# Kernel tuning notes

Hardware: AMD Instinct MI355X
Metric: run time of the kernel (lower is better)

## Reference

```python
import jax, jax.numpy as jnp
import numpy as np

IC = 256   # inter_channels
CIN = 512  # in_channels == out_channels
HOP = 3
EPS = 1e-5


def conv1x1(x, w, b):
    # x: [B,C,H,W], w: [O,C], b: [O]
    return jnp.einsum('bchw,oc->bohw', x, w) + b[None, :, None, None]


def bn_eval(x, g, beta, mean, var):
    inv = g / jnp.sqrt(var + EPS)
    return x * inv[None, :, None, None] + (beta - mean * inv)[None, :, None, None]


def setup_inputs() -> dict:
    key = jax.random.key(0)
    ks = jax.random.split(key, 12)
    s = lambda *sh: 0.02
    inp = {
        'x': jax.random.normal(ks[0], (4, CIN, 64, 64), dtype=jnp.float32),
        'delta': jnp.array([0.5], dtype=jnp.float32),
        'w1_w': jax.random.normal(ks[1], (IC, CIN), dtype=jnp.float32) * 0.02,
        'w1_b': jnp.zeros((IC,), jnp.float32),
        'bn1_g': jnp.ones((IC,), jnp.float32),
        'bn1_b': jnp.zeros((IC,), jnp.float32),
        'bn1_m': jnp.zeros((IC,), jnp.float32),
        'bn1_v': jnp.ones((IC,), jnp.float32),
        'node_w': jax.random.normal(ks[2], (IC, CIN), dtype=jnp.float32) * 0.02,
        'node_b': jnp.zeros((IC,), jnp.float32),
        'hop_w': jax.random.normal(ks[3], (HOP, IC, IC), dtype=jnp.float32) * 0.02,
        'hop_b': jnp.zeros((HOP, IC), jnp.float32),
        'fuse_w': jax.random.normal(ks[4], (IC, HOP * IC), dtype=jnp.float32) * 0.02,
        'fuse_b': jnp.zeros((IC,), jnp.float32),
        'bnf_g': jnp.ones((IC,), jnp.float32),
        'bnf_b': jnp.zeros((IC,), jnp.float32),
        'bnf_m': jnp.zeros((IC,), jnp.float32),
        'bnf_v': jnp.ones((IC,), jnp.float32),
        'res_w': jax.random.normal(ks[5], (CIN, 2 * IC), dtype=jnp.float32) * 0.02,
        'res_b': jnp.zeros((CIN,), jnp.float32),
        'bnr_g': jnp.ones((CIN,), jnp.float32),
        'bnr_b': jnp.zeros((CIN,), jnp.float32),
        'bnr_m': jnp.zeros((CIN,), jnp.float32),
        'bnr_v': jnp.ones((CIN,), jnp.float32),
    }
    return inp


def reference(x, delta, w1_w, w1_b, bn1_g, bn1_b, bn1_m, bn1_v,
              node_w, node_b, hop_w, hop_b, fuse_w, fuse_b,
              bnf_g, bnf_b, bnf_m, bnf_v, res_w, res_b,
              bnr_g, bnr_b, bnr_m, bnr_v):
    B, C, H, W = x.shape
    N = H * W
    # w1_conv == w2_conv (shared weights in the original module)
    wfeat = bn_eval(conv1x1(x, w1_w, w1_b), bn1_g, bn1_b, bn1_m, bn1_v)  # [B,IC,H,W]
    wflat = wfeat.reshape(B, IC, N)
    # initial_w = w1^T @ w2, scaled: [B,N,N]
    iw = jnp.einsum('bcn,bcm->bnm', wflat, wflat) * (IC ** -0.5)
    nodes = conv1x1(x, node_w, node_b).reshape(B, IC, N).transpose(0, 2, 1)  # [B,N,IC]
    # thresholded binary mask (non-differentiable, as in torch .ge)
    b0 = (jax.nn.sigmoid(iw) - delta[0] >= 0.0).astype(iw.dtype)
    bh = b0
    hops = []
    for i in range(HOP):
        s = jax.nn.softmax(bh * iw, axis=-1)          # [B,N,N]
        t = jnp.einsum('bnm,bmc->bnc', s, nodes)      # [B,N,IC]
        t = t.transpose(0, 2, 1).reshape(B, IC, H, W)
        t = conv1x1(t, hop_w[i], hop_b[i])
        hops.append(t)
        if i != HOP - 1:
            bh = jnp.matmul(bh, b0)                   # binary adjacency power
    x_p = jnp.concatenate(hops, axis=1)               # [B,HOP*IC,H,W]
    x_p = bn_eval(conv1x1(x_p, fuse_w, fuse_b), bnf_g, bnf_b, bnf_m, bnf_v)
    out = jnp.concatenate((wfeat * 0 + wfeat, x_p), axis=1) if False else jnp.concatenate((x_pad(x), x_p), axis=1)
    out = bn_eval(conv1x1(out, res_w, res_b), bnr_g, bnr_b, bnr_m, bnr_v)
    return out


def x_pad(x):
    # note: res_conv expects 2*IC input channels; original concatenates x (in_channels)
    # with x_p (inter_channels). With in_channels=512 and IC=256 the torch module as
    # written requires in_channels + IC == 2*IC only if in_channels == IC; the repo's
    # res_conv takes 2*inter_channels, so faithfully we feed x projected? No -- the
    # original concatenates raw x. To keep channel math consistent with the declared
    # Conv2d(2*IC, out), we slice x to IC channels (matches runnable configuration).
    return x[:, :IC]
```

## Files before the change

### kernel.cpp

```cpp
#include <hip/hip_runtime.h>

#define CINCH 512
#define ICH 256
#define NP 4096
#define BB 4
#define GSTRIDE ((size_t)NP*16)

typedef __attribute__((ext_vector_type(8))) short bf16x8;
typedef __attribute__((ext_vector_type(8))) unsigned short u16x8;
typedef __attribute__((ext_vector_type(4))) float f32x4;
typedef __attribute__((ext_vector_type(4))) int i32x4;
typedef unsigned short u16;
typedef unsigned char u8;
typedef unsigned long long u64;

__device__ __forceinline__ u16 f2bf(float f){
  unsigned u = __builtin_bit_cast(unsigned, f);
  u += 0x7FFFu + ((u>>16)&1u);
  return (u16)(u>>16);
}

__device__ __forceinline__ float b0_thr(float dv){
  if (dv <= 0.f) return -3.4e38f;
  if (dv >= 1.f) return  3.4e38f;
  return (float)log((double)dv/(1.0-(double)dv));
}

__device__ __forceinline__ size_t fragaddr(int row, int k){
  return (size_t)(row>>4)*GSTRIDE + (size_t)(k>>4)*256 + (size_t)((row&15)*16 + (k&15));
}
__device__ __forceinline__ size_t fragidx(int row, int col){
  return ((size_t)(row>>4)*(NP>>4) + (size_t)(col>>4))*256 + (size_t)((row&15)*16 + (col&15));
}
__device__ __forceinline__ size_t ndfrag(int ic, int n){
  return ((size_t)(ic>>4)*(NP>>5) + (size_t)(n>>5))*512
       + (size_t)((ic&15)*32 + ((n>>3)&3)*8 + (n&7));
}

__global__ __launch_bounds__(256) void k_proj(const float* __restrict__ x,
    const float* __restrict__ w1w, const float* __restrict__ w1b,
    const float* __restrict__ g1, const float* __restrict__ be1,
    const float* __restrict__ mu1, const float* __restrict__ va1,
    const float* __restrict__ nw, const float* __restrict__ nb,
    float* __restrict__ Wt, u16* __restrict__ ndT){
  const int b = blockIdx.z;
  const int n0 = blockIdx.x*64, c0 = blockIdx.y*64;
  const int t = threadIdx.x, tx=t&15, ty=t>>4;
  __shared__ float as_[32][68];
  __shared__ float w1T[32][68];
  __shared__ float w2T[32][68];
  double acc1d[4][4];
  float acc1[4][4], acc2[4][4];
  #pragma unroll
  for(int i=0;i<4;i++)
    #pragma unroll
    for(int j=0;j<4;j++){acc1d[i][j]=0.0; acc1[i][j]=0.f; acc2[i][j]=0.f;}
  const float* xb = x + (size_t)b*CINCH*NP;
  for(int cb=0; cb<CINCH; cb+=32){
    __syncthreads();
    #pragma unroll
    for(int h=0;h<2;h++){
      int f = t + h*256;
      {
        int row=f>>4, c4=f&15;
        float4 v=*(const float4*)(xb + (size_t)(cb+row)*NP + n0 + c4*4);
        *(float4*)&as_[row][c4*4] = v;
      }
      {
        int k=f&31, ocq=f>>5;
        float l1[4], l2[4];
        #pragma unroll
        for(int r=0;r<4;r++){
          l1[r]=w1w[(size_t)(c0+ocq*4+r)*CINCH + cb + k];
          l2[r]=nw [(size_t)(c0+ocq*4+r)*CINCH + cb + k];
        }
        *(float4*)&w1T[k][ocq*4] = *(float4*)l1;
        *(float4*)&w2T[k][ocq*4] = *(float4*)l2;
      }
    }
    __syncthreads();
    #pragma unroll
    for(int k=0;k<32;k++){
      float4 av=*(const float4*)&as_[k][ty*4];
      float4 b1=*(const float4*)&w1T[k][tx*4];
      float4 b2=*(const float4*)&w2T[k][tx*4];
      float avf[4]={av.x,av.y,av.z,av.w};
      float b1f[4]={b1.x,b1.y,b1.z,b1.w};
      float b2f[4]={b2.x,b2.y,b2.z,b2.w};
      #pragma unroll
      for(int i=0;i<4;i++)
        #pragma unroll
        for(int j=0;j<4;j++){
          acc1[i][j] = fmaf(avf[i], b1f[j], acc1[i][j]);
          acc2[i][j] = fmaf(avf[i], b2f[j], acc2[i][j]);
        }
    }
    #pragma unroll
    for(int i=0;i<4;i++)
      #pragma unroll
      for(int j=0;j<4;j++){ acc1d[i][j] += (double)acc1[i][j]; acc1[i][j]=0.f; }
  }
  float inv[4], add[4], b1v[4], b2v[4];
  #pragma unroll
  for(int j=0;j<4;j++){
    int c=c0+tx*4+j;
    inv[j]=g1[c]*rsqrtf(va1[c]+1e-5f);
    add[j]=be1[c]-mu1[c]*inv[j];
    b1v[j]=w1b[c]; b2v[j]=nb[c];
  }
  #pragma unroll
  for(int i=0;i<4;i++){
    int n=n0+ty*4+i;
    float4 ov;
    float o[4];
    #pragma unroll
    for(int j=0;j<4;j++) o[j]=((float)(acc1d[i][j]+(double)b1v[j]))*inv[j]+add[j];
    ov.x=o[0];ov.y=o[1];ov.z=o[2];ov.w=o[3];
    *(float4*)(Wt + ((size_t)b*NP + n)*ICH + c0+tx*4) = ov;
  }
  u16* ndTb = ndT + (size_t)b*ICH*NP;
  #pragma unroll
  for(int j=0;j<4;j++){
    int ic=c0+tx*4+j;
    ushort4 uv;
    uv.x=f2bf(acc2[0][j]+b2v[j]); uv.y=f2bf(acc2[1][j]+b2v[j]);
    uv.z=f2bf(acc2[2][j]+b2v[j]); uv.w=f2bf(acc2[3][j]+b2v[j]);
    *(ushort4*)(ndTb + ndfrag(ic, n0+ty*4)) = uv;
  }
}

__global__ __launch_bounds__(256) void k_iw(const float* __restrict__ Wb,
    float* __restrict__ ob, u8* __restrict__ b0f, const float* __restrict__ delta){
  int tt = blockIdx.x;
  tt = (tt&7)*260 + (tt>>3);
  int bi = (int)((sqrtf(8.f*(float)tt+1.f)-1.f)*0.5f);
  while(bi*(bi+1)/2 > tt) bi--;
  while((bi+1)*(bi+2)/2 <= tt) bi++;
  int bj = tt - bi*(bi+1)/2;
  const int r0=bi*64, c0=bj*64;
  const float thr = b0_thr(delta[0]);
  __shared__ float asT[32][68], bsT[32][68];
  const int t=threadIdx.x, tx=t&15, ty=t>>4;
  double accd[4][4];
  float accf[4][4];
  #pragma unroll
  for(int i=0;i<4;i++)
    #pragma unroll
    for(int j=0;j<4;j++){accd[i][j]=0.0; accf[i][j]=0.f;}
  for(int k0=0;k0<ICH;k0+=32){
    __syncthreads();
    {
      int r=t>>3, kv=(t&7)*4;
      #pragma unroll
      for(int rr=r; rr<64; rr+=32){
        float4 va=*(const float4*)(Wb + (size_t)(r0+rr)*ICH + k0+kv);
        asT[kv+0][rr]=va.x; asT[kv+1][rr]=va.y; asT[kv+2][rr]=va.z; asT[kv+3][rr]=va.w;
        float4 vb=*(const float4*)(Wb + (size_t)(c0+rr)*ICH + k0+kv);
        bsT[kv+0][rr]=vb.x; bsT[kv+1][rr]=vb.y; bsT[kv+2][rr]=vb.z; bsT[kv+3][rr]=vb.w;
      }
    }
    __syncthreads();
    #pragma unroll
    for(int k=0;k<32;k++){
      float4 av=*(const float4*)&asT[k][ty*4];
      float4 bv=*(const float4*)&bsT[k][tx*4];
      float avf[4]={av.x,av.y,av.z,av.w};
      float bvf[4]={bv.x,bv.y,bv.z,bv.w};
      #pragma unroll
      for(int i=0;i<4;i++)
        #pragma unroll
        for(int j=0;j<4;j++)
          accf[i][j] = fmaf(avf[i], bvf[j], accf[i][j]);
    }
    #pragma unroll
    for(int i=0;i<4;i++)
      #pragma unroll
      for(int j=0;j<4;j++){ accd[i][j] += (double)accf[i][j]; accf[i][j]=0.f; }
  }
  float vv[4][4];
  char bvs[4][4];
  #pragma unroll
  for(int i=0;i<4;i++)
    #pragma unroll
    for(int j=0;j<4;j++){
      float v = (float)(accd[i][j]*0.0625);
      vv[i][j]=v;
      bvs[i][j]= v>=thr ? 1 : 0;
    }
  #pragma unroll
  for(int i=0;i<4;i++){
    float4 ov; ov.x=vv[i][0];ov.y=vv[i][1];ov.z=vv[i][2];ov.w=vv[i][3];
    *(float4*)(ob + fragidx(r0+ty*4+i, c0+tx*4)) = ov;
    unsigned w = (u8)bvs[i][0] | ((u8)bvs[i][1]<<8) | ((u8)bvs[i][2]<<16) | ((u8)bvs[i][3]<<24);
    *(unsigned*)(b0f + fragaddr(r0+ty*4+i, c0+tx*4)) = w;
  }
  if(bi!=bj){
    #pragma unroll
    for(int j=0;j<4;j++){
      float4 ov; ov.x=vv[0][j];ov.y=vv[1][j];ov.z=vv[2][j];ov.w=vv[3][j];
      *(float4*)(ob + fragidx(c0+tx*4+j, r0+ty*4)) = ov;
      unsigned w = (u8)bvs[0][j] | ((u8)bvs[1][j]<<8) | ((u8)bvs[2][j]<<16) | ((u8)bvs[3][j]<<24);
      *(unsigned*)(b0f + fragaddr(c0+tx*4+j, r0+ty*4)) = w;
    }
  }
}

__global__ __launch_bounds__(256) void k_nn0(const u8* __restrict__ b0f,
    u8* __restrict__ bh1lo, u8* __restrict__ bh1hi){
  int tt = blockIdx.x;
  tt = (tt&7)*66 + (tt>>3);
  int bi = (int)((sqrtf(8.f*(float)tt+1.f)-1.f)*0.5f);
  while(bi*(bi+1)/2 > tt) bi--;
  while((bi+1)*(bi+2)/2 <= tt) bi++;
  int bj = tt - bi*(bi+1)/2;
  const int r0=bi*128, c0=bj*128;
  const int t=threadIdx.x, w=t>>6, l=t&63;
  const int wr=(w>>1)*64, wc=(w&1)*64, fr=l&15, fg=l>>4;
  const i32x4 zer={0,0,0,0};
  i32x4 acc[4][4];
  #pragma unroll
  for(int i=0;i<4;i++)
    #pragma unroll
    for(int j=0;j<4;j++) acc[i][j]=zer;
  const size_t aoff = (size_t)fr*16 + (size_t)fg*256;
  const u8* pA[4]; const u8* pB[4];
  #pragma unroll
  for(int mi=0;mi<4;mi++) pA[mi]=b0f + (size_t)(((r0+wr)>>4) + mi)*GSTRIDE + aoff;
  #pragma unroll
  for(int nj=0;nj<4;nj++) pB[nj]=b0f + (size_t)(((c0+wc)>>4) + nj)*GSTRIDE + aoff;
  for(int k0=0;k0<NP;k0+=64){
    const size_t idx=(size_t)k0*16;
    i32x4 af[4], bf_[4];
    #pragma unroll
    for(int mi=0;mi<4;mi++) af[mi]=*(const i32x4*)(pA[mi]+idx);
    #pragma unroll
    for(int nj=0;nj<4;nj++) bf_[nj]=*(const i32x4*)(pB[nj]+idx);
    #pragma unroll
    for(int mi=0;mi<4;mi++)
      #pragma unroll
      for(int nj=0;nj<4;nj++)
        acc[mi][nj]=__builtin_amdgcn_mfma_i32_16x16x64_i8(af[mi],bf_[nj],acc[mi][nj],0,0,0);
  }
  #pragma unroll
  for(int mi=0;mi<4;mi++){
    #pragma unroll
    for(int nj=0;nj<4;nj++){
      int gc=c0+wc+nj*16+fr;
      int grb=r0+wr+mi*16+fg*4;
      u8 lob[4], hib[4];
      #pragma unroll
      for(int r=0;r<4;r++){
        int v=acc[mi][nj][r];
        lob[r]=(u8)(v&127); hib[r]=(u8)(v>>7);
        size_t ad=fragaddr(grb+r,gc);
        bh1lo[ad]=lob[r];
        bh1hi[ad]=hib[r];
      }
      if(bi!=bj){
        unsigned wlo = (unsigned)lob[0] | ((unsigned)lob[1]<<8) | ((unsigned)lob[2]<<16) | ((unsigned)lob[3]<<24);
        unsigned whi = (unsigned)hib[0] | ((unsigned)hib[1]<<8) | ((unsigned)hib[2]<<16) | ((unsigned)hib[3]<<24);
        size_t ad=fragaddr(gc,grb);
        *(unsigned*)(bh1lo+ad)=wlo;
        *(unsigned*)(bh1hi+ad)=whi;
      }
    }
  }
}

__global__ __launch_bounds__(256) void k_nn1(const u8* __restrict__ bh1lo,
    const u8* __restrict__ bh1hi, const u8* __restrict__ b0f,
    u16* __restrict__ bh2lo, u8* __restrict__ bh2hi){
  int tt = blockIdx.x;
  tt = (tt&7)*66 + (tt>>3);
  int bi = (int)((sqrtf(8.f*(float)tt+1.f)-1.f)*0.5f);
  while(bi*(bi+1)/2 > tt) bi--;
  while((bi+1)*(bi+2)/2 <= tt) bi++;
  int bj = tt - bi*(bi+1)/2;
  const int r0=bi*128, c0=bj*128;
  const int t=threadIdx.x, w=t>>6, l=t&63;
  const int wr=(w>>1)*64, wc=(w&1)*64, fr=l&15, fg=l>>4;
  const i32x4 zer={0,0,0,0};
  i32x4 acc[4][4];
  #pragma unroll
  for(int i=0;i<4;i++)
    #pragma unroll
    for(int j=0;j<4;j++) acc[i][j]=zer;
  const size_t aoff = (size_t)fr*16 + (size_t)fg*256;
  const u8* pAlo[4]; const u8* pAhi[4]; const u8* pB[4];
  #pragma unroll
  for(int mi=0;mi<4;mi++){
    size_t g = (size_t)(((r0+wr)>>4) + mi)*GSTRIDE + aoff;
    pAlo[mi]=bh1lo+g; pAhi[mi]=bh1hi+g;
  }
  #pragma unroll
  for(int nj=0;nj<4;nj++)
    pB[nj]=b0f + (size_t)(((c0+wc)>>4) + nj)*GSTRIDE + aoff;
  for(int k0=0;k0<NP;k0+=64){
    const size_t idx=(size_t)k0*16;
    i32x4 ah[4], bf_[4];
    #pragma unroll
    for(int mi=0;mi<4;mi++) ah[mi]=*(const i32x4*)(pAhi[mi]+idx);
    #pragma unroll
    for(int nj=0;nj<4;nj++) bf_[nj]=*(const i32x4*)(pB[nj]+idx);
    #pragma unroll
    for(int mi=0;mi<4;mi++)
      #pragma unroll
      for(int nj=0;nj<4;nj++)
        acc[mi][nj]=__builtin_amdgcn_mfma_i32_16x16x64_i8(ah[mi],bf_[nj],acc[mi][nj],0,0,0);
  }
  #pragma unroll
  for(int mi=0;mi<4;mi++)
    #pragma unroll
    for(int nj=0;nj<4;nj++)
      #pragma unroll
      for(int r=0;r<4;r++) acc[mi][nj][r] <<= 7;
  for(int k0=0;k0<NP;k0+=64){
    const size_t idx=(size_t)k0*16;
    i32x4 al[4], bf_[4];
    #pragma unroll
    for(int mi=0;mi<4;mi++) al[mi]=*(const i32x4*)(pAlo[mi]+idx);
    #pragma unroll
    for(int nj=0;nj<4;nj++) bf_[nj]=*(const i32x4*)(pB[nj]+idx);
    #pragma unroll
    for(int mi=0;mi<4;mi++)
      #pragma unroll
      for(int nj=0;nj<4;nj++)
        acc[mi][nj]=__builtin_amdgcn_mfma_i32_16x16x64_i8(al[mi],bf_[nj],acc[mi][nj],0,0,0);
  }
  #pragma unroll
  for(int mi=0;mi<4;mi++){
    #pragma unroll
    for(int nj=0;nj<4;nj++){
      int gr=r0+wr+mi*16+fg*4, gc=c0+wc+nj*16+fr;
      u16 ml[4]; u8 mh[4];
      #pragma unroll
      for(int r=0;r<4;r++){
        int v = acc[mi][nj][r];
        u16 lo=(u16)(v & 0xFFFF); u8 hi=(u8)(v>>16);
        ml[r]=lo; mh[r]=hi;
        size_t ad = fragidx(gr+r, gc);
        bh2lo[ad]=lo; bh2hi[ad]=hi;
      }
      if(bi!=bj){
        size_t ad = fragidx(gc, gr);
        *(ushort4*)(bh2lo + ad) = *(ushort4*)ml;
        *(unsigned*)(bh2hi + ad) = (unsigned)mh[0] | ((unsigned)mh[1]<<8)
                                 | ((unsigned)mh[2]<<16) | ((unsigned)mh[3]<<24);
      }
    }
  }
}

template<int H>
__device__ __forceinline__ void pv_body(const float* __restrict__ iw,
    const u8* __restrict__ bh1lo, const u8* __restrict__ bh1hi,
    const u16* __restrict__ bh2lo, const u8* __restrict__ bh2hi,
    const u16* __restrict__ ndT, const float* __restrict__ delta,
    float* __restrict__ traw, int rs,
    float (*Lm)[16], float (*Ls)[16], float (*Lacc)[16][4][64]){
  const int t = threadIdx.x, w = t>>6, l = t&63, fr = l&15, fg = l>>4;
  const int kbase = w*1024;
  const float thr = b0_thr(delta[0]);
  const f32x4 zer={0.f,0.f,0.f,0.f};
  f32x4 acc[16];
  #pragma unroll
  for(int i=0;i<16;i++) acc[i]=zer;
  float m_run=-3.0e38f, s_run=0.f;
  const size_t af32 = ((size_t)rs*(NP>>4) + (size_t)(kbase>>4) + (fg>>1))*256
                    + (size_t)(fr*16 + (fg&1)*8);
  const float* ipf = iw + af32;
  const u16* p2lo = bh2lo + af32;
  const u8*  p2hi = bh2hi + af32;
  const u8* plo = bh1lo + af32;
  const u8* phi = bh1hi + af32;
  const size_t nb0 = (size_t)(kbase>>5)*512 + (size_t)(fr*32 + fg*8);
  for(int k0=0;k0<1024;k0+=32){
    const size_t idxf = (size_t)(k0>>4)*256;
    const size_t idxn = (size_t)k0*16;
    bf16x8 bfr[16];
    #pragma unroll
    for(int nj=0;nj<16;nj++)
      bfr[nj]=*(const bf16x8*)(ndT + (size_t)nj*65536 + nb0 + idxn);
    float vv[8];
    {
      float4 v0=*(const float4*)(ipf+idxf), v1=*(const float4*)(ipf+idxf+4);
      vv[0]=v0.x; vv[1]=v0.y; vv[2]=v0.z; vv[3]=v0.w;
      vv[4]=v1.x; vv[5]=v1.y; vv[6]=v1.z; vv[7]=v1.w;
    }
    float lg[8];
    if(H==0){
      #pragma unroll
      for(int e=0;e<8;e++) lg[e]=vv[e]>=thr?vv[e]:0.f;
    } else if(H==1){
      u64 llo=*(const u64*)(plo + idxf);
      u64 lhi=*(const u64*)(phi + idxf);
      #pragma unroll
      for(int e=0;e<8;e++){
        int bh_ = (int)((llo>>(8*e))&255u) | ((int)((lhi>>(8*e))&255u)<<7);
        lg[e]=(float)bh_*vv[e];
      }
    } else {
      u16x8 lv=*(const u16x8*)(p2lo + idxf);
      u64   hv=*(const u64*)(p2hi + idxf);
      #pragma unroll
      for(int e=0;e<8;e++){
        int v = (int)(unsigned short)lv[e] | ((int)((hv>>(8*e))&255u)<<16);
        lg[e]=(float)v*vv[e];
      }
    }
    float m_t = fmaxf(fmaxf(fmaxf(lg[0],lg[1]),fmaxf(lg[2],lg[3])),
                      fmaxf(fmaxf(lg[4],lg[5]),fmaxf(lg[6],lg[7])));
    m_t = fmaxf(m_t, __shfl_xor(m_t,16));
    m_t = fmaxf(m_t, __shfl_xor(m_t,32));
    if(__any(m_t > m_run + 6.0f)){
      float m_new = fmaxf(m_run, m_t);
      float sc = __expf(m_run - m_new);
      s_run *= sc;
      #pragma unroll
      for(int r=0;r<4;r++){
        float scr = __shfl(sc, fg*4+r);
        #pragma unroll
        for(int nj=0;nj<16;nj++) acc[nj][r]*=scr;
      }
      m_run = m_new;
    }
    bf16x8 af; float ss=0.f;
    #pragma unroll
    for(int e=0;e<8;e++){
      float p=__expf(lg[e]-m_run); ss+=p;
      af[e]=(short)f2bf(p);
    }
    s_run += ss;
    #pragma unroll
    for(int nj=0;nj<16;nj++)
      acc[nj]=__builtin_amdgcn_mfma_f32_16x16x32_bf16(af,bfr[nj],acc[nj],0,0,0);
  }
  s_run += __shfl_xor(s_run,16);
  s_run += __shfl_xor(s_run,32);
  if(fg==0) Lm[w][fr]=m_run;
  __syncthreads();
  float f_c[4];
  #pragma unroll
  for(int r=0;r<4;r++){
    int rr=fg*4+r;
    float ms=fmaxf(fmaxf(Lm[0][rr],Lm[1][rr]),fmaxf(Lm[2][rr],Lm[3][rr]));
    f_c[r]=__expf(Lm[w][rr]-ms);
  }
  {
    float ms=fmaxf(fmaxf(Lm[0][fr],Lm[1][fr]),fmaxf(Lm[2][fr],Lm[3][fr]));
    float fs=__expf(Lm[w][fr]-ms);
    if(fg==0) Ls[w][fr]=s_run*fs;
  }
  #pragma unroll
  for(int nj=0;nj<16;nj++)
    #pragma unroll
    for(int r=0;r<4;r++) acc[nj][r]*=f_c[r];
  if(w==1||w==3){
    int Ri=(w==1)?0:1;
    #pragma unroll
    for(int nj=0;nj<16;nj++)
      #pragma unroll
      for(int r=0;r<4;r++) Lacc[Ri][nj][r][l]=acc[nj][r];
  }
  __syncthreads();
  if(w==0||w==2){
    int Ri=(w==0)?0:1;
    #pragma unroll
    for(int nj=0;nj<16;nj++)
      #pragma unroll
      for(int r=0;r<4;r++) acc[nj][r]+=Lacc[Ri][nj][r][l];
  }
  __syncthreads();
  if(w==2){
    #pragma unroll
    for(int nj=0;nj<16;nj++)
      #pragma unroll
      for(int r=0;r<4;r++) Lacc[0][nj][r][l]=acc[nj][r];
  }
  __syncthreads();
  if(w==0){
    float sst[4];
    #pragma unroll
    for(int r=0;r<4;r++){
      int rr=fg*4+r;
      sst[r]=1.0f/(Ls[0][rr]+Ls[1][rr]+Ls[2][rr]+Ls[3][rr]);
    }
    #pragma unroll
    for(int nj=0;nj<16;nj++)
      #pragma unroll
      for(int r=0;r<4;r++){
        float v=(acc[nj][r]+Lacc[0][nj][r][l])*sst[r];
        traw[(size_t)(rs*16+fg*4+r)*ICH + nj*16+fr]=v;
      }
  }
}

__global__ __launch_bounds__(256) void k_pv3(const float* __restrict__ iw,
    const u8* __restrict__ bh1lo, const u8* __restrict__ bh1hi,
    const u16* __restrict__ bh2lo, const u8* __restrict__ bh2hi,
    const u16* __restrict__ ndT, const float* __restrict__ delta,
    float* __restrict__ trawcat){
  __shared__ float Lm[4][16], Ls[4][16];
  __shared__ float Lacc[2][16][4][64];
  int idx = blockIdx.x;
  idx = (idx&7)*96 + (idx>>3);
  const int rs = idx/3, h = idx - rs*3;
  float* traw = trawcat + (size_t)h*NP*ICH;
  if(h==0)      pv_body<0>(iw,bh1lo,bh1hi,bh2lo,bh2hi,ndT,delta,traw,rs,Lm,Ls,Lacc);
  else if(h==1) pv_body<1>(iw,bh1lo,bh1hi,bh2lo,bh2hi,ndT,delta,traw,rs,Lm,Ls,Lacc);
  else          pv_body<2>(iw,bh1lo,bh1hi,bh2lo,bh2hi,ndT,delta,traw,rs,Lm,Ls,Lacc);
}

__global__ __launch_bounds__(256) void k_prepA(const float* __restrict__ fw,
    const float* __restrict__ hw, const float* __restrict__ hb,
    const float* __restrict__ fb,
    const float* __restrict__ gf, const float* __restrict__ bef,
    const float* __restrict__ muf, const float* __restrict__ vaf,
    float* __restrict__ G, float* __restrict__ cf,
    float* __restrict__ sf, float* __restrict__ tf){
  const int t=threadIdx.x;
  if(blockIdx.x<768){
    int i=blockIdx.x>>8, oc=blockIdx.x&255;
    float s=0.f;
    const float* fr_=fw + (size_t)oc*768 + i*256;
    const float* hp=hw + (size_t)i*ICH*ICH + t;
    for(int j=0;j<256;j++) s=fmaf(fr_[j], hp[(size_t)j*ICH], s);
    G[((size_t)i*ICH + oc)*ICH + t]=s;
  } else {
    float iv=gf[t]*rsqrtf(vaf[t]+1e-5f);
    sf[t]=iv;
    tf[t]=bef[t]-muf[t]*iv;
    float s=fb[t];
    const float* fr_=fw + (size_t)t*768;
    for(int k=0;k<768;k++) s=fmaf(fr_[k], hb[k], s);
    cf[t]=s;
  }
}

__global__ __launch_bounds__(256) void k_prepB(const float* __restrict__ rw,
    const float* __restrict__ rb, const float* __restrict__ G,
    const float* __restrict__ cf, const float* __restrict__ sf,
    const float* __restrict__ tf, float* __restrict__ Wcat,
    float* __restrict__ evec){
  const int oc=blockIdx.x, t=threadIdx.x;
  __shared__ float rs_[256], rw2_[256];
  rw2_[t]=rw[(size_t)oc*512 + 256 + t];
  rs_[t]=rw2_[t]*sf[t];
  __syncthreads();
  Wcat[(size_t)oc*1024 + t] = rw[(size_t)oc*512 + t];
  #pragma unroll
  for(int i=0;i<3;i++){
    float s=0.f;
    const float* gp=G + (size_t)i*ICH*ICH + t;
    for(int m=0;m<256;m++) s=fmaf(rs_[m], gp[(size_t)m*ICH], s);
    Wcat[(size_t)oc*1024 + 256 + i*256 + t]=s;
  }
  if(t==0){
    float s=rb[oc];
    for(int m=0;m<256;m++) s=fmaf(rs_[m],cf[m],s)+rw2_[m]*tf[m];
    evec[oc]=s;
  }
}

__global__ __launch_bounds__(256) void k_tail2(const float* __restrict__ trawcat,
    const float* __restrict__ Wcat, const float* __restrict__ evec,
    const float* __restrict__ xsrc,
    const float* __restrict__ g, const float* __restrict__ be,
    const float* __restrict__ mu, const float* __restrict__ va,
    float* __restrict__ Cout){
  const int n0=blockIdx.x*64, c0=blockIdx.y*64;
  __shared__ float asT[32][68], bsT[32][68];
  const int t=threadIdx.x, tx=t&15, ty=t>>4;
  float acc[4][4];
  #pragma unroll
  for(int i=0;i<4;i++)
    #pragma unroll
    for(int j=0;j<4;j++) acc[i][j]=0.f;
  for(int k0=0;k0<1024;k0+=32){
    __syncthreads();
    if(k0<256){
      int kk=t>>4, nv=(t&15)*4;
      #pragma unroll
      for(int k2=kk;k2<32;k2+=16)
        *(float4*)&asT[k2][nv] = *(const float4*)(xsrc + (size_t)(k0+k2)*NP + n0+nv);
    } else {
      int hop=(k0-256)>>8, kk0=(k0-256)&255;
      const float* A=trawcat + (size_t)hop*NP*ICH;
      int r=t>>3, kv=(t&7)*4;
      #pragma unroll
      for(int rr=r;rr<64;rr+=32){
        float4 v=*(const float4*)(A + (size_t)(n0+rr)*ICH + kk0+kv);
        asT[kv+0][rr]=v.x; asT[kv+1][rr]=v.y; asT[kv+2][rr]=v.z; asT[kv+3][rr]=v.w;
      }
    }
    {
      int r=t>>3, kv=(t&7)*4;
      #pragma unroll
      for(int rr=r;rr<64;rr+=32){
        float4 v=*(const float4*)(Wcat + (size_t)(c0+rr)*1024 + k0+kv);
        bsT[kv+0][rr]=v.x; bsT[kv+1][rr]=v.y; bsT[kv+2][rr]=v.z; bsT[kv+3][rr]=v.w;
      }
    }
    __syncthreads();
    #pragma unroll
    for(int k=0;k<32;k++){
      float4 av=*(const float4*)&asT[k][ty*4];
      float4 bv=*(const float4*)&bsT[k][tx*4];
      float avf[4]={av.x,av.y,av.z,av.w};
      float bvf[4]={bv.x,bv.y,bv.z,bv.w};
      #pragma unroll
      for(int i=0;i<4;i++)
        #pragma unroll
        for(int j=0;j<4;j++) acc[i][j]+=avf[i]*bvf[j];
    }
  }
  const int col=c0+tx*4, row=n0+ty*4;
  float sc[4], ad[4];
  #pragma unroll
  for(int j=0;j<4;j++){
    int c=col+j;
    float iv=g[c]*rsqrtf(va[c]+1e-5f);
    sc[j]=iv; ad[j]=be[c]-mu[c]*iv + evec[c]*iv;
  }
  #pragma unroll
  for(int j=0;j<4;j++){
    float4 ov;
    ov.x=acc[0][j]*sc[j]+ad[j]; ov.y=acc[1][j]*sc[j]+ad[j];
    ov.z=acc[2][j]*sc[j]+ad[j]; ov.w=acc[3][j]*sc[j]+ad[j];
    *(float4*)(Cout + (size_t)(col+j)*NP + row) = ov;
  }
}

__global__ void k_diag(float* out, int n, float val){
  int i = blockIdx.x*256 + threadIdx.x;
  if(i<n) out[i] = (i==0)? val : 0.f;
}

extern "C" void kernel_launch(void* const* d_in, const int* in_sizes, int n_in,
                              void* d_out, int out_size, void* d_ws, size_t ws_size,
                              hipStream_t stream){
  const float* x    =(const float*)d_in[0];
  const float* delta=(const float*)d_in[1];
  const float* w1w  =(const float*)d_in[2];
  const float* w1b  =(const float*)d_in[3];
  const float* g1   =(const float*)d_in[4];
  const float* be1  =(const float*)d_in[5];
  const float* mu1  =(const float*)d_in[6];
  const float* va1  =(const float*)d_in[7];
  const float* nw   =(const float*)d_in[8];
  const float* nb   =(const float*)d_in[9];
  const float* hw   =(const float*)d_in[10];
  const float* hb   =(const float*)d_in[11];
  const float* fw   =(const float*)d_in[12];
  const float* fb   =(const float*)d_in[13];
  const float* gf   =(const float*)d_in[14];
  const float* bef  =(const float*)d_in[15];
  const float* muf  =(const float*)d_in[16];
  const float* vaf  =(const float*)d_in[17];
  const float* rw   =(const float*)d_in[18];
  const float* rb   =(const float*)d_in[19];
  const float* gr   =(const float*)d_in[20];
  const float* ber  =(const float*)d_in[21];
  const float* mur  =(const float*)d_in[22];
  const float* var_ =(const float*)d_in[23];
  float* out=(float*)d_out;

  char* ws=(char*)d_ws;
  size_t o=0;
  auto alloc=[&](size_t bytes)->char*{ char* p=ws+o; o+=(bytes+255)&~(size_t)255; return p; };
  const size_t NN=(size_t)NP*NP;
  float* Wt    =(float*)alloc((size_t)BB*NP*ICH*4);
  u16*   ndT   =(u16*)  alloc((size_t)BB*ICH*NP*2);
  float* iw    =(float*)alloc(NN*4);
  u8*    b0f   =(u8*)   alloc(NN);
  u8*    bh1lo =(u8*)   alloc(NN);
  u8*    bh1hi =(u8*)   alloc(NN);
  u16*   bh2lo =(u16*)  alloc(NN*2);
  u8*    bh2hi =(u8*)   alloc(NN);
  float* trawc =(float*)alloc((size_t)3*NP*ICH*4);
  float* G     =(float*)alloc((size_t)3*ICH*ICH*4);
  float* Wcat  =(float*)alloc((size_t)CINCH*1024*4);
  float* evec  =(float*)alloc(CINCH*4);
  float* cf    =(float*)alloc(ICH*4);
  float* sf    =(float*)alloc(ICH*4);
  float* tf    =(float*)alloc(ICH*4);
  if(o > ws_size){
    k_diag<<<dim3((out_size+255)/256),dim3(256),0,stream>>>(out, out_size, (float)ws_size);
    return;
  }
  dim3 blk(256);
  k_prepA<<<dim3(769),blk,0,stream>>>(fw,hw,hb,fb,gf,bef,muf,vaf,G,cf,sf,tf);
  k_prepB<<<dim3(512),blk,0,stream>>>(rw,rb,G,cf,sf,tf,Wcat,evec);
  k_proj<<<dim3(NP/64,ICH/64,BB),blk,0,stream>>>(x,w1w,w1b,g1,be1,mu1,va1,nw,nb,Wt,ndT);
  for(int b=0;b<BB;b++){
    const float* Wt_b  = Wt + (size_t)b*NP*ICH;
    const u16*   ndT_b = ndT + (size_t)b*ICH*NP;
    const float* x_b   = x + (size_t)b*CINCH*NP;
    float*       out_b = out + (size_t)b*CINCH*NP;
    k_iw  <<<dim3(2080),blk,0,stream>>>(Wt_b,iw,b0f,delta);
    k_nn0 <<<dim3(528),blk,0,stream>>>(b0f,bh1lo,bh1hi);
    k_nn1 <<<dim3(528),blk,0,stream>>>(bh1lo,bh1hi,b0f,bh2lo,bh2hi);
    k_pv3 <<<dim3(768),blk,0,stream>>>(iw,bh1lo,bh1hi,bh2lo,bh2hi,ndT_b,delta,trawc);
    k_tail2<<<dim3(64,8),blk,0,stream>>>(trawc,Wcat,evec,x_b,gr,ber,mur,var_,out_b);
  }
}
```

Measured before the change: 2.277 ms.

## Stage adjacency tiles in LDS and merge lo/hi int8 MFMA passes

The k_nn1 adjacency-power kernel now cooperatively loads the A-lo, A-hi and B fragments for each 64-deep K step into shared memory. Each wave then reads its fragments from LDS instead of issuing redundant global loads, since waves in the same block share rows and columns. The two separate K loops for the high and low bytes are fused into one loop with two accumulator sets that are combined at the end. This reduces global traffic and reuses the B loads, but doubles accumulator registers, which may lower occupancy, and adds two barriers per iteration without double buffering.

```diff
diff --git a/kernel.cpp b/kernel.cpp
--- a/kernel.cpp
+++ b/kernel.cpp
@@ -279,53 +279,44 @@
   const int r0=bi*128, c0=bj*128;
   const int t=threadIdx.x, w=t>>6, l=t&63;
   const int wr=(w>>1)*64, wc=(w&1)*64, fr=l&15, fg=l>>4;
+  __shared__ __align__(16) u8 sAlo[8192];
+  __shared__ __align__(16) u8 sAhi[8192];
+  __shared__ __align__(16) u8 sB[8192];
   const i32x4 zer={0,0,0,0};
-  i32x4 acc[4][4];
+  i32x4 accl[4][4], acch[4][4];
   #pragma unroll
   for(int i=0;i<4;i++)
     #pragma unroll
-    for(int j=0;j<4;j++) acc[i][j]=zer;
-  const size_t aoff = (size_t)fr*16 + (size_t)fg*256;
-  const u8* pAlo[4]; const u8* pAhi[4]; const u8* pB[4];
-  #pragma unroll
-  for(int mi=0;mi<4;mi++){
-    size_t g = (size_t)(((r0+wr)>>4) + mi)*GSTRIDE + aoff;
-    pAlo[mi]=bh1lo+g; pAhi[mi]=bh1hi+g;
-  }
-  #pragma unroll
-  for(int nj=0;nj<4;nj++)
-    pB[nj]=b0f + (size_t)(((c0+wc)>>4) + nj)*GSTRIDE + aoff;
+    for(int j=0;j<4;j++){accl[i][j]=zer; acch[i][j]=zer;}
+  const int rg=t>>5; const int gb=(t&31)*32;
+  const size_t gA = (size_t)((r0>>4)+rg)*GSTRIDE + gb;
+  const size_t gB = (size_t)((c0>>4)+rg)*GSTRIDE + gb;
+  const int lofs = fg*256 + fr*16;
   for(int k0=0;k0<NP;k0+=64){
-    const size_t idx=(size_t)k0*16;
-    i32x4 ah[4], bf_[4];
-    #pragma unroll
-    for(int mi=0;mi<4;mi++) ah[mi]=*(const i32x4*)(pAhi[mi]+idx);
-    #pragma unroll
-    for(int nj=0;nj<4;nj++) bf_[nj]=*(const i32x4*)(pB[nj]+idx);
+    __syncthreads();
+    const size_t ko=(size_t)(k0>>4)*256;
+    *(float4*)&sAlo[rg*1024+gb]    = *(const float4*)(bh1lo+gA+ko);
+    *(float4*)&sAlo[rg*1024+gb+16] = *(const float4*)(bh1lo+gA+ko+16);
+    *(float4*)&sAhi[rg*1024+gb]    = *(const float4*)(bh1hi+gA+ko);
+    *(float4*)&sAhi[rg*1024+gb+16] = *(const float4*)(bh1hi+gA+ko+16);
+    *(float4*)&sB[rg*1024+gb]      = *(const float4*)(b0f+gB+ko);
+    *(float4*)&sB[rg*1024+gb+16]   = *(const float4*)(b0f+gB+ko+16);
+    __syncthreads();
+    i32x4 al[4], ah[4], bf_[4];
+    #pragma unroll
+    for(int mi=0;mi<4;mi++){
+      al[mi]=*(const i32x4*)&sAlo[((wr>>4)+mi)*1024+lofs];
+      ah[mi]=*(const i32x4*)&sAhi[((wr>>4)+mi)*1024+lofs];
+    }
+    #pragma unroll
+    for(int nj=0;nj<4;nj++) bf_[nj]=*(const i32x4*)&sB[((wc>>4)+nj)*1024+lofs];
     #pragma unroll
     for(int mi=0;mi<4;mi++)
       #pragma unroll
-      for(int nj=0;nj<4;nj++)
-        acc[mi][nj]=__builtin_amdgcn_mfma_i32_16x16x64_i8(ah[mi],bf_[nj],acc[mi][nj],0,0,0);
-  }
-  #pragma unroll
-  for(int mi=0;mi<4;mi++)
-    #pragma unroll
-    for(int nj=0;nj<4;nj++)
-      #pragma unroll
-      for(int r=0;r<4;r++) acc[mi][nj][r] <<= 7;
-  for(int k0=0;k0<NP;k0+=64){
-    const size_t idx=(size_t)k0*16;
-    i32x4 al[4], bf_[4];
-    #pragma unroll
-    for(int mi=0;mi<4;mi++) al[mi]=*(const i32x4*)(pAlo[mi]+idx);
-    #pragma unroll
-    for(int nj=0;nj<4;nj++) bf_[nj]=*(const i32x4*)(pB[nj]+idx);
-    #pragma unroll
-    for(int mi=0;mi<4;mi++)
-      #pragma unroll
-      for(int nj=0;nj<4;nj++)
-        acc[mi][nj]=__builtin_amdgcn_mfma_i32_16x16x64_i8(al[mi],bf_[nj],acc[mi][nj],0,0,0);
+      for(int nj=0;nj<4;nj++){
+        accl[mi][nj]=__builtin_amdgcn_mfma_i32_16x16x64_i8(al[mi],bf_[nj],accl[mi][nj],0,0,0);
+        acch[mi][nj]=__builtin_amdgcn_mfma_i32_16x16x64_i8(ah[mi],bf_[nj],acch[mi][nj],0,0,0);
+      }
   }
   #pragma unroll
   for(int mi=0;mi<4;mi++){
@@ -335,7 +326,7 @@
       u16 ml[4]; u8 mh[4];
       #pragma unroll
       for(int r=0;r<4;r++){
-        int v = acc[mi][nj][r];
+        int v = accl[mi][nj][r] + (acch[mi][nj][r]<<7);
         u16 lo=(u16)(v & 0xFFFF); u8 hi=(u8)(v>>16);
         ml[r]=lo; mh[r]=hi;
         size_t ad = fragidx(gr+r, gc);
```

Result: slower. 2.419 ms (+6.2%).

## Retile symmetric adjacency-power matmul into 128x256 strip tiles plus diagonal kernel

Applied to the files above, without the earlier changes.

Replaces the triangular 128x128 tile schedule of the second adjacency-power int8 matmul with 128x256 tiles covering strictly-lower pairs of column blocks, launched as 256 blocks. A separate 16-block kernel handles the even diagonal 128x128 tiles. Wider tiles raise reuse of the A operand per loaded B fragment and cut block count and scheduling overhead. The cost is more accumulator registers per thread (128 i32 values), which may lower occupancy, and a more involved tile-index mapping.

```diff
diff --git a/kernel.cpp b/kernel.cpp
--- a/kernel.cpp
+++ b/kernel.cpp
@@ -267,70 +267,64 @@
   }
 }
 
-__global__ __launch_bounds__(256) void k_nn1(const u8* __restrict__ bh1lo,
+__global__ __launch_bounds__(256) void k_nn1p(const u8* __restrict__ bh1lo,
     const u8* __restrict__ bh1hi, const u8* __restrict__ b0f,
     u16* __restrict__ bh2lo, u8* __restrict__ bh2hi){
-  int tt = blockIdx.x;
-  tt = (tt&7)*66 + (tt>>3);
-  int bi = (int)((sqrtf(8.f*(float)tt+1.f)-1.f)*0.5f);
-  while(bi*(bi+1)/2 > tt) bi--;
-  while((bi+1)*(bi+2)/2 <= tt) bi++;
-  int bj = tt - bi*(bi+1)/2;
-  const int r0=bi*128, c0=bj*128;
+  int idx = blockIdx.x;
+  idx = (idx&7)*32 + (idx>>3);
+  int bi = (int)(2.f*sqrtf((float)idx)) + 1;
+  if(bi>32) bi=32;
+  while(((bi*bi-(bi&1))>>2) > idx) bi--;
+  while((((bi+1)*(bi+1)-((bi+1)&1))>>2) <= idx) bi++;
+  const int p = idx - ((bi*bi-(bi&1))>>2);
+  const int r0 = bi*128, c0 = p*256;
   const int t=threadIdx.x, w=t>>6, l=t&63;
-  const int wr=(w>>1)*64, wc=(w&1)*64, fr=l&15, fg=l>>4;
+  const int wr=(w>>1)*64, wc=(w&1)*128, fr=l&15, fg=l>>4;
   const i32x4 zer={0,0,0,0};
-  i32x4 acc[4][4];
+  i32x4 acc[4][8];
   #pragma unroll
   for(int i=0;i<4;i++)
     #pragma unroll
-    for(int j=0;j<4;j++) acc[i][j]=zer;
+    for(int j=0;j<8;j++) acc[i][j]=zer;
   const size_t aoff = (size_t)fr*16 + (size_t)fg*256;
-  const u8* pAlo[4]; const u8* pAhi[4]; const u8* pB[4];
-  #pragma unroll
-  for(int mi=0;mi<4;mi++){
-    size_t g = (size_t)(((r0+wr)>>4) + mi)*GSTRIDE + aoff;
-    pAlo[mi]=bh1lo+g; pAhi[mi]=bh1hi+g;
-  }
-  #pragma unroll
-  for(int nj=0;nj<4;nj++)
-    pB[nj]=b0f + (size_t)(((c0+wc)>>4) + nj)*GSTRIDE + aoff;
+  const size_t gAlo = (size_t)((r0+wr)>>4)*GSTRIDE + aoff;
+  const size_t gB   = (size_t)((c0+wc)>>4)*GSTRIDE + aoff;
   for(int k0=0;k0<NP;k0+=64){
-    const size_t idx=(size_t)k0*16;
-    i32x4 ah[4], bf_[4];
-    #pragma unroll
-    for(int mi=0;mi<4;mi++) ah[mi]=*(const i32x4*)(pAhi[mi]+idx);
-    #pragma unroll
-    for(int nj=0;nj<4;nj++) bf_[nj]=*(const i32x4*)(pB[nj]+idx);
+    const size_t kk=(size_t)k0*16;
+    i32x4 ah[4], bf_[8];
+    #pragma unroll
+    for(int mi=0;mi<4;mi++) ah[mi]=*(const i32x4*)(bh1hi + gAlo + (size_t)mi*GSTRIDE + kk);
+    #pragma unroll
+    for(int nj=0;nj<8;nj++) bf_[nj]=*(const i32x4*)(b0f + gB + (size_t)nj*GSTRIDE + kk);
     #pragma unroll
     for(int mi=0;mi<4;mi++)
       #pragma unroll
-      for(int nj=0;nj<4;nj++)
+      for(int nj=0;nj<8;nj++)
         acc[mi][nj]=__builtin_amdgcn_mfma_i32_16x16x64_i8(ah[mi],bf_[nj],acc[mi][nj],0,0,0);
   }
   #pragma unroll
   for(int mi=0;mi<4;mi++)
     #pragma unroll
-    for(int nj=0;nj<4;nj++)
+    for(int nj=0;nj<8;nj++)
       #pragma unroll
       for(int r=0;r<4;r++) acc[mi][nj][r] <<= 7;
   for(int k0=0;k0<NP;k0+=64){
-    const size_t idx=(size_t)k0*16;
-    i32x4 al[4], bf_[4];
-    #pragma unroll
-    for(int mi=0;mi<4;mi++) al[mi]=*(const i32x4*)(pAlo[mi]+idx);
-    #pragma unroll
-    for(int nj=0;nj<4;nj++) bf_[nj]=*(const i32x4*)(pB[nj]+idx);
+    const size_t kk=(size_t)k0*16;
+    i32x4 al[4], bf_[8];
+    #pragma unroll
+    for(int mi=0;mi<4;mi++) al[mi]=*(const i32x4*)(bh1lo + gAlo + (size_t)mi*GSTRIDE + kk);
+    #pragma unroll
+    for(int nj=0;nj<8;nj++) bf_[nj]=*(const i32x4*)(b0f + gB + (size_t)nj*GSTRIDE + kk);
     #pragma unroll
     for(int mi=0;mi<4;mi++)
       #pragma unroll
-      for(int nj=0;nj<4;nj++)
+      for(int nj=0;nj<8;nj++)
         acc[mi][nj]=__builtin_amdgcn_mfma_i32_16x16x64_i8(al[mi],bf_[nj],acc[mi][nj],0,0,0);
   }
   #pragma unroll
   for(int mi=0;mi<4;mi++){
     #pragma unroll
-    for(int nj=0;nj<4;nj++){
+    for(int nj=0;nj<8;nj++){
       int gr=r0+wr+mi*16+fg*4, gc=c0+wc+nj*16+fr;
       u16 ml[4]; u8 mh[4];
       #pragma unroll
@@ -341,11 +335,76 @@
         size_t ad = fragidx(gr+r, gc);
         bh2lo[ad]=lo; bh2hi[ad]=hi;
       }
-      if(bi!=bj){
+      {
         size_t ad = fragidx(gc, gr);
         *(ushort4*)(bh2lo + ad) = *(ushort4*)ml;
         *(unsigned*)(bh2hi + ad) = (unsigned)mh[0] | ((unsigned)mh[1]<<8)
                                  | ((unsigned)mh[2]<<16) | ((unsigned)mh[3]<<24);
+      }
+    }
+  }
+}
+
+__global__ __launch_bounds__(256) void k_nn1d(const u8* __restrict__ bh1lo,
+    const u8* __restrict__ bh1hi, const u8* __restrict__ b0f,
+    u16* __restrict__ bh2lo, u8* __restrict__ bh2hi){
+  int idx = blockIdx.x;
+  idx = (idx&7)*2 + (idx>>3);
+  const int bi = idx*2;
+  const int r0=bi*128, c0=bi*128;
+  const int t=threadIdx.x, w=t>>6, l=t&63;
+  const int wr=(w>>1)*64, wc=(w&1)*64, fr=l&15, fg=l>>4;
+  const i32x4 zer={0,0,0,0};
+  i32x4 acc[4][4];
+  #pragma unroll
+  for(int i=0;i<4;i++)
+    #pragma unroll
+    for(int j=0;j<4;j++) acc[i][j]=zer;
+  const size_t aoff = (size_t)fr*16 + (size_t)fg*256;
+  const size_t gA = (size_t)((r0+wr)>>4)*GSTRIDE + aoff;
+  const size_t gB = (size_t)((c0+wc)>>4)*GSTRIDE + aoff;
+  for(int k0=0;k0<NP;k0+=64){
+    const size_t kk=(size_t)k0*16;
+    i32x4 ah[4], bf_[4];
+    #pragma unroll
+    for(int mi=0;mi<4;mi++) ah[mi]=*(const i32x4*)(bh1hi + gA + (size_t)mi*GSTRIDE + kk);
+    #pragma unroll
+    for(int nj=0;nj<4;nj++) bf_[nj]=*(const i32x4*)(b0f + gB + (size_t)nj*GSTRIDE + kk);
+    #pragma unroll
+    for(int mi=0;mi<4;mi++)
+      #pragma unroll
+      for(int nj=0;nj<4;nj++)
+        acc[mi][nj]=__builtin_amdgcn_mfma_i32_16x16x64_i8(ah[mi],bf_[nj],acc[mi][nj],0,0,0);
+  }
+  #pragma unroll
+  for(int mi=0;mi<4;mi++)
+    #pragma unroll
+    for(int nj=0;nj<4;nj++)
+      #pragma unroll
+      for(int r=0;r<4;r++) acc[mi][nj][r] <<= 7;
+  for(int k0=0;k0<NP;k0+=64){
+    const size_t kk=(size_t)k0*16;
+    i32x4 al[4], bf_[4];
+    #pragma unroll
+    for(int mi=0;mi<4;mi++) al[mi]=*(const i32x4*)(bh1lo + gA + (size_t)mi*GSTRIDE + kk);
+    #pragma unroll
+    for(int nj=0;nj<4;nj++) bf_[nj]=*(const i32x4*)(b0f + gB + (size_t)nj*GSTRIDE + kk);
+    #pragma unroll
+    for(int mi=0;mi<4;mi++)
+      #pragma unroll
+      for(int nj=0;nj<4;nj++)
+        acc[mi][nj]=__builtin_amdgcn_mfma_i32_16x16x64_i8(al[mi],bf_[nj],acc[mi][nj],0,0,0);
+  }
+  #pragma unroll
+  for(int mi=0;mi<4;mi++){
+    #pragma unroll
+    for(int nj=0;nj<4;nj++){
+      int gr=r0+wr+mi*16+fg*4, gc=c0+wc+nj*16+fr;
+      #pragma unroll
+      for(int r=0;r<4;r++){
+        int v = acc[mi][nj][r];
+        size_t ad = fragidx(gr+r, gc);
+        bh2lo[ad]=(u16)(v & 0xFFFF); bh2hi[ad]=(u8)(v>>16);
       }
     }
   }
@@ -699,7 +758,8 @@
     float*       out_b = out + (size_t)b*CINCH*NP;
     k_iw  <<<dim3(2080),blk,0,stream>>>(Wt_b,iw,b0f,delta);
     k_nn0 <<<dim3(528),blk,0,stream>>>(b0f,bh1lo,bh1hi);
-    k_nn1 <<<dim3(528),blk,0,stream>>>(bh1lo,bh1hi,b0f,bh2lo,bh2hi);
+    k_nn1p<<<dim3(256),blk,0,stream>>>(bh1lo,bh1hi,b0f,bh2lo,bh2hi);
+    k_nn1d<<<dim3(16),blk,0,stream>>>(bh1lo,bh1hi,b0f,bh2lo,bh2hi);
     k_pv3 <<<dim3(768),blk,0,stream>>>(iw,bh1lo,bh1hi,bh2lo,bh2hi,ndT_b,delta,trawc);
     k_tail2<<<dim3(64,8),blk,0,stream>>>(trawc,Wcat,evec,x_b,gr,ber,mur,var_,out_b);
   }
```

New measurement: 2.415 ms. 6.1% more time.
